# Optimization experiments

Hardware: AMD Instinct MI355X
Metric: run time of the kernel (lower is better)

Reference implementation:

```python
import jax, jax.numpy as jnp
import numpy as np

N_NODES = 100000
N_EDGES = 3200000
N_FEAT = 512
HIDDEN = 16
N_CLASS = 7


def gcn_conv(x, edge_index, W, b, n_nodes):
    """PyG GCNConv (add_self_loops=True, symmetric normalization).
    x: [N, F_in]; edge_index: [2, E] with row=source, col=target.
    """
    h = x @ W  # [N, F_out] -- linear transform before aggregation (F_out small)
    src, dst = edge_index[0], edge_index[1]
    # degree computed on target column (incl. self-loop), as in PyG gcn_norm
    deg = jax.ops.segment_sum(jnp.ones(src.shape[0], dtype=h.dtype), dst,
                              num_segments=n_nodes) + 1.0
    dinv = jax.lax.rsqrt(deg)  # deg >= 1 always (self-loops)
    norm = dinv[src] * dinv[dst]  # [E]
    msg = norm[:, None] * h[src]  # [E, F_out]
    agg = jax.ops.segment_sum(msg, dst, num_segments=n_nodes)
    # self-loop contribution: norm_ii = dinv_i^2
    agg = agg + (dinv * dinv)[:, None] * h
    return agg + b


def setup_inputs() -> dict:
    key = jax.random.key(0)
    k1, k2, k3, k4 = jax.random.split(key, 4)
    x = jax.random.normal(k1, (N_NODES, N_FEAT), dtype=jnp.float32)
    edge_index = jax.random.randint(k2, (2, N_EDGES), 0, N_NODES, dtype=jnp.int64)
    W1 = jax.random.normal(k3, (N_FEAT, HIDDEN), dtype=jnp.float32) * (1.0 / np.sqrt(N_FEAT))
    b1 = jnp.zeros((HIDDEN,), dtype=jnp.float32)
    W2 = jax.random.normal(k4, (HIDDEN, N_CLASS), dtype=jnp.float32) * (1.0 / np.sqrt(HIDDEN))
    b2 = jnp.zeros((N_CLASS,), dtype=jnp.float32)
    return {"x": x, "edge_index": edge_index, "W1": W1, "b1": b1, "W2": W2, "b2": b2}


def reference(x, edge_index, W1, b1, W2, b2):
    n = x.shape[0]
    h = gcn_conv(x, edge_index, W1, b1, n)
    h = jax.nn.relu(h)
    # F.dropout in eval mode is identity (deterministic reference)
    h = gcn_conv(h, edge_index, W2, b2, n)
    return jax.nn.log_softmax(h, axis=1)
```

## Files before the change

### kernel.cpp

```cpp
#include <hip/hip_runtime.h>
#include <math.h>


#define F_IN 512
#define HID  16
#define NCLS 7
#define NCHUNK 256
#define BK 256
#define NBMAX 400
#define CAP 9216
#define WT_STRIDE 516

static __device__ __forceinline__ float bf2f(unsigned short u) {
    union { unsigned int i; float f; } v; v.i = ((unsigned int)u) << 16; return v.f;
}
static __device__ __forceinline__ unsigned short f2bf(float f) {
    union { float f; unsigned int u; } v; v.f = f;
    unsigned int b = v.u;
    return (unsigned short)((b + 0x7FFFu + ((b >> 16) & 1u)) >> 16);
}

__global__ __launch_bounds__(256) void k_a1(const int* __restrict__ ei, int E, int perChunk,
                                            int nb, int* __restrict__ bh) {
    __shared__ int hist[NBMAX];
    for (int t = threadIdx.x; t < nb; t += 256) hist[t] = 0;
    __syncthreads();
    const int* dst = ei + E;
    int c = blockIdx.x;
    int s0 = c * perChunk;
    int s1 = min(s0 + perChunk, E);
    for (int e = s0 + threadIdx.x; e < s1; e += 256)
        atomicAdd(&hist[dst[e] >> 8], 1);
    __syncthreads();
    for (int t = threadIdx.x; t < nb; t += 256) bh[(size_t)c * nb + t] = hist[t];
}

__global__ __launch_bounds__(256) void k_a2a(int* __restrict__ bh, int nb,
                                             int* __restrict__ Tb) {
    __shared__ int sd[256];
    int b = blockIdx.x, tid = threadIdx.x;
    int v = bh[(size_t)tid * nb + b];
    sd[tid] = v;
    __syncthreads();
    for (int off = 1; off < 256; off <<= 1) {
        int t = (tid >= off) ? sd[tid - off] : 0;
        __syncthreads();
        sd[tid] += t;
        __syncthreads();
    }
    bh[(size_t)tid * nb + b] = sd[tid] - v;
    if (tid == 255) Tb[b] = sd[255];
}

__global__ __launch_bounds__(256) void k_a2b(const int* __restrict__ Tb, int nb,
                                             int* __restrict__ Bb) {
    __shared__ int sd[256];
    int tid = threadIdx.x;
    int carry = 0;
    for (int base = 0; base < nb; base += 256) {
        int v = (base + tid < nb) ? Tb[base + tid] : 0;
        sd[tid] = v;
        __syncthreads();
        for (int off = 1; off < 256; off <<= 1) {
            int t = (tid >= off) ? sd[tid - off] : 0;
            __syncthreads();
            sd[tid] += t;
            __syncthreads();
        }
        if (base + tid < nb) Bb[base + tid] = carry + sd[tid] - v;
        carry += sd[255];
        __syncthreads();
    }
}

__global__ __launch_bounds__(256) void k_a3(const int* __restrict__ ei, int E, int perChunk,
                                            int nb, const int* __restrict__ bh,
                                            const int* __restrict__ Bb,
                                            unsigned* __restrict__ part) {
    __shared__ int cur[NBMAX];
    __shared__ int baseL[NBMAX];
    int c = blockIdx.x;
    for (int t = threadIdx.x; t < nb; t += 256) {
        cur[t] = 0;
        baseL[t] = Bb[t] + bh[(size_t)c * nb + t];
    }
    __syncthreads();
    const int* src = ei;
    const int* dst = ei + E;
    int s0 = c * perChunk;
    int s1 = min(s0 + perChunk, E);
    for (int e = s0 + threadIdx.x; e < s1; e += 256) {
        int s = src[e], d = dst[e];
        int b = d >> 8;
        int r = atomicAdd(&cur[b], 1);
        part[baseL[b] + r] = ((unsigned)(d & (BK - 1)) << 20) | (unsigned)s;
    }
}

__global__ __launch_bounds__(256) void k_b(const unsigned* __restrict__ part,
                                           const int* __restrict__ Tb,
                                           const int* __restrict__ Bb,
                                           int* __restrict__ csr, int* __restrict__ cnt,
                                           int* __restrict__ offs, float* __restrict__ dinv,
                                           int N) {
    __shared__ unsigned eL[CAP];
    __shared__ int hist[BK], sd[BK], cur[BK];
    int b = blockIdx.x, tid = threadIdx.x;
    int base = Bb[b], ct = Tb[b];
    hist[tid] = 0;
    __syncthreads();
    for (int k = tid; k < ct; k += 256) {
        unsigned v = part[base + k];
        if (k < CAP) eL[k] = v;
        atomicAdd(&hist[v >> 20], 1);
    }
    __syncthreads();
    sd[tid] = hist[tid];
    __syncthreads();
    for (int off = 1; off < BK; off <<= 1) {
        int t = (tid >= off) ? sd[tid - off] : 0;
        __syncthreads();
        sd[tid] += t;
        __syncthreads();
    }
    {
        int h = hist[tid];
        int ex = sd[tid] - h;
        cur[tid] = ex;
        int node = b * BK + tid;
        if (node < N) {
            cnt[node] = h;
            offs[node] = base + ex;
            dinv[node] = rsqrtf((float)h + 1.0f);
        }
    }
    __syncthreads();
    for (int k = tid; k < ct; k += 256) {
        unsigned v = (k < CAP) ? eL[k] : part[base + k];
        int dl = (int)(v >> 20);
        int r = atomicAdd(&cur[dl], 1);
        csr[base + r] = (int)(v & 0xFFFFFu);
    }
}

__global__ __launch_bounds__(256) void k_gemm1(const float* __restrict__ x,
                                               const float* __restrict__ W1,
                                               const float* __restrict__ dinv,
                                               unsigned short* __restrict__ hs1b,
                                               int N) {
    __shared__ float wlT[HID * WT_STRIDE];

    int lane = threadIdx.x & 15;
    int g = threadIdx.x >> 4;
    int rbase = blockIdx.x * 64 + g * 4;

    const float* xp0 = x + (size_t)(rbase + 0 < N ? rbase + 0 : 0) * F_IN + 4 * lane;
    const float* xp1 = x + (size_t)(rbase + 1 < N ? rbase + 1 : 0) * F_IN + 4 * lane;
    const float* xp2 = x + (size_t)(rbase + 2 < N ? rbase + 2 : 0) * F_IN + 4 * lane;
    const float* xp3 = x + (size_t)(rbase + 3 < N ? rbase + 3 : 0) * F_IN + 4 * lane;

    float4 a0 = *(const float4*)(xp0);
    float4 a1 = *(const float4*)(xp1);
    float4 a2 = *(const float4*)(xp2);
    float4 a3 = *(const float4*)(xp3);

    {
        int j = threadIdx.x & 15;
        int k0 = threadIdx.x >> 4;
        for (int it = 0; it < F_IN / 16; ++it) {
            int k = k0 + 16 * it;
            wlT[j * WT_STRIDE + k] = W1[k * HID + j];
        }
    }
    __syncthreads();

    float acc[4][16];
#pragma unroll
    for (int r = 0; r < 4; ++r)
#pragma unroll
        for (int j = 0; j < 16; ++j) acc[r][j] = 0.0f;

    auto fma_block = [&](int p, const float4& A0, const float4& A1,
                         const float4& A2, const float4& A3) {
        const float* wb = &wlT[64 * p + 4 * lane];
#pragma unroll
        for (int j = 0; j < 16; ++j) {
            float4 w4 = *(const float4*)(wb + (size_t)j * WT_STRIDE);
            acc[0][j] = fmaf(A0.x, w4.x, fmaf(A0.y, w4.y, fmaf(A0.z, w4.z, fmaf(A0.w, w4.w, acc[0][j]))));
            acc[1][j] = fmaf(A1.x, w4.x, fmaf(A1.y, w4.y, fmaf(A1.z, w4.z, fmaf(A1.w, w4.w, acc[1][j]))));
            acc[2][j] = fmaf(A2.x, w4.x, fmaf(A2.y, w4.y, fmaf(A2.z, w4.z, fmaf(A2.w, w4.w, acc[2][j]))));
            acc[3][j] = fmaf(A3.x, w4.x, fmaf(A3.y, w4.y, fmaf(A3.z, w4.z, fmaf(A3.w, w4.w, acc[3][j]))));
        }
    };

#pragma unroll 1
    for (int p = 0; p < 7; ++p) {
        float4 n0 = *(const float4*)(xp0 + 64 * (p + 1));
        float4 n1 = *(const float4*)(xp1 + 64 * (p + 1));
        float4 n2 = *(const float4*)(xp2 + 64 * (p + 1));
        float4 n3 = *(const float4*)(xp3 + 64 * (p + 1));
        fma_block(p, a0, a1, a2, a3);
        a0 = n0; a1 = n1; a2 = n2; a3 = n3;
    }
    fma_block(7, a0, a1, a2, a3);

    bool b8 = (lane & 8) != 0, b4 = (lane & 4) != 0, b2 = (lane & 2) != 0, b1 = (lane & 1) != 0;
#pragma unroll
    for (int r = 0; r < 4; ++r) {
#pragma unroll
        for (int j = 0; j < 8; ++j) {
            float lo = acc[r][j], hi = acc[r][j + 8];
            float keep = b8 ? hi : lo;
            float send = b8 ? lo : hi;
            acc[r][j] = keep + __shfl_xor(send, 8, 16);
        }
#pragma unroll
        for (int j = 0; j < 4; ++j) {
            float lo = acc[r][j], hi = acc[r][j + 4];
            float keep = b4 ? hi : lo;
            float send = b4 ? lo : hi;
            acc[r][j] = keep + __shfl_xor(send, 4, 16);
        }
#pragma unroll
        for (int j = 0; j < 2; ++j) {
            float lo = acc[r][j], hi = acc[r][j + 2];
            float keep = b2 ? hi : lo;
            float send = b2 ? lo : hi;
            acc[r][j] = keep + __shfl_xor(send, 2, 16);
        }
        {
            float lo = acc[r][0], hi = acc[r][1];
            float keep = b1 ? hi : lo;
            float send = b1 ? lo : hi;
            acc[r][0] = keep + __shfl_xor(send, 1, 16);
        }
        int row = rbase + r;
        if (row < N)
            hs1b[(size_t)row * HID + lane] = f2bf(dinv[row] * acc[r][0]);
    }
}

__global__ __launch_bounds__(256) void k_agg1(const int* __restrict__ csr,
                                              const int* __restrict__ offs,
                                              const int* __restrict__ cnt,
                                              const float* __restrict__ dinv,
                                              const unsigned* __restrict__ hs1u,
                                              const float* __restrict__ b1,
                                              const float* __restrict__ W2,
                                              float* __restrict__ hs2p, int N) {
    int lane = threadIdx.x & 7;
    int i = blockIdx.x * 32 + (threadIdx.x >> 3);
    float w2a[NCLS], w2b[NCLS];
#pragma unroll
    for (int c = 0; c < NCLS; c++) {
        w2a[c] = W2[(2 * lane) * NCLS + c];
        w2b[c] = W2[(2 * lane + 1) * NCLS + c];
    }
    float b1a = b1[2 * lane], b1b = b1[2 * lane + 1];
    if (i >= N) return;
    int start = offs[i], cn = cnt[i];
    unsigned su = hs1u[(size_t)i * 8 + lane];
    float accA = __uint_as_float(su << 16);
    float accB = __uint_as_float(su & 0xffff0000u);
    int full = cn & ~7;
    int rem = cn - full;
    int evn = csr[start + lane];
    for (int k = 0; k < full; k += 8) {
        int ev = evn;
        evn = csr[start + k + 8 + lane];
#pragma unroll
        for (int t = 0; t < 8; ++t) {
            int s = __shfl(ev, t, 8);
            unsigned u = hs1u[(size_t)s * 8 + lane];
            accA += __uint_as_float(u << 16);
            accB += __uint_as_float(u & 0xffff0000u);
        }
    }
    for (int t = 0; t < rem; ++t) {
        int s = __shfl(evn, t, 8);
        unsigned u = hs1u[(size_t)s * 8 + lane];
        accA += __uint_as_float(u << 16);
        accB += __uint_as_float(u & 0xffff0000u);
    }
    float dv = dinv[i];
    float vA = fmaf(dv, accA, b1a);
    float vB = fmaf(dv, accB, b1b);
    float hA = vA > 0.0f ? vA : 0.0f;
    float hB = vB > 0.0f ? vB : 0.0f;
    float res[NCLS];
#pragma unroll
    for (int c = 0; c < NCLS; c++) {
        float t = fmaf(hA, w2a[c], hB * w2b[c]);
#pragma unroll
        for (int w = 4; w >= 1; w >>= 1) t += __shfl_xor(t, w, 8);
        res[c] = t;
    }
    float o = res[0];
#pragma unroll
    for (int c = 1; c < NCLS; c++) o = (lane == c) ? res[c] : o;
    hs2p[(size_t)i * 8 + lane] = dv * o;
}

__global__ __launch_bounds__(256) void k_agg2(const int* __restrict__ csr,
                                              const int* __restrict__ offs,
                                              const int* __restrict__ cnt,
                                              const float* __restrict__ dinv,
                                              const float* __restrict__ hs2p,
                                              const float* __restrict__ b2,
                                              float* __restrict__ out, int N) {
    int lane = threadIdx.x & 7;
    int i = blockIdx.x * 32 + (threadIdx.x >> 3);
    if (i >= N) return;
    int start = offs[i], cn = cnt[i];
    float acc = hs2p[(size_t)i * 8 + lane];
    int full = cn & ~7;
    int rem = cn - full;
    int evn = csr[start + lane];
    for (int k = 0; k < full; k += 8) {
        int ev = evn;
        evn = csr[start + k + 8 + lane];
#pragma unroll
        for (int t = 0; t < 8; ++t) {
            int s = __shfl(ev, t, 8);
            acc += hs2p[(size_t)s * 8 + lane];
        }
    }
    for (int t = 0; t < rem; ++t) {
        int s = __shfl(evn, t, 8);
        acc += hs2p[(size_t)s * 8 + lane];
    }
    int cc = lane < NCLS ? lane : NCLS - 1;
    float v = fmaf(dinv[i], acc, b2[cc]);
    float vm = (lane < NCLS) ? v : -INFINITY;
    float m = vm;
#pragma unroll
    for (int w = 4; w >= 1; w >>= 1) m = fmaxf(m, __shfl_xor(m, w, 8));
    float e = (lane < NCLS) ? expf(v - m) : 0.0f;
    float ssum = e;
#pragma unroll
    for (int w = 4; w >= 1; w >>= 1) ssum += __shfl_xor(ssum, w, 8);
    if (lane < NCLS) out[(size_t)i * NCLS + lane] = v - m - logf(ssum);
}

extern "C" void kernel_launch(void* const* d_in, const int* in_sizes, int n_in,
                              void* d_out, int out_size, void* d_ws, size_t ws_size,
                              hipStream_t stream) {
    const float* x  = (const float*)d_in[0];
    const int*   ei = (const int*)d_in[1];
    const float* W1 = (const float*)d_in[2];
    const float* b1 = (const float*)d_in[3];
    const float* W2 = (const float*)d_in[4];
    const float* b2 = (const float*)d_in[5];
    float* out = (float*)d_out;

    const int N = in_sizes[0] / F_IN;
    const int E = in_sizes[1] / 2;
    const int nb = (N + BK - 1) / BK;
    const int perChunk = (E + NCHUNK - 1) / NCHUNK;

    unsigned* w = (unsigned*)d_ws;
    auto al4 = [](size_t v) { return (v + 3) & ~(size_t)3; };
    size_t o = 0;
    unsigned*       part = w + o;
    float*          hs2p = (float*)(w + o);     o = al4(o + E);
    int*            csr  = (int*)(w + o);       o = al4(o + E + 16);
    unsigned short* hs1b = (unsigned short*)(w + o); o = al4(o + (size_t)N * HID / 2);
    float*          dinv = (float*)(w + o);     o = al4(o + N);
    int*            cnt  = (int*)(w + o);       o = al4(o + N);
    int*            offs = (int*)(w + o);       o = al4(o + N);
    int*            bh   = (int*)(w + o);       o = al4(o + (size_t)NCHUNK * nb);
    int*            Tb   = (int*)(w + o);       o = al4(o + nb);
    int*            Bb   = (int*)(w + o);

    k_a1<<<NCHUNK, 256, 0, stream>>>(ei, E, perChunk, nb, bh);
    k_a2a<<<nb, 256, 0, stream>>>(bh, nb, Tb);
    k_a2b<<<1, 256, 0, stream>>>(Tb, nb, Bb);
    k_a3<<<NCHUNK, 256, 0, stream>>>(ei, E, perChunk, nb, bh, Bb, part);
    k_b<<<nb, 256, 0, stream>>>(part, Tb, Bb, csr, cnt, offs, dinv, N);
    k_gemm1<<<(N + 63) / 64, 256, 0, stream>>>(x, W1, dinv, hs1b, N);
    k_agg1<<<(N + 31) / 32, 256, 0, stream>>>(csr, offs, cnt, dinv,
                                              (const unsigned*)hs1b, b1, W2, hs2p, N);
    k_agg2<<<(N + 31) / 32, 256, 0, stream>>>(csr, offs, cnt, dinv, hs2p, b2, out, N);
}
```

Before: 448.5 us.

## Overlap the dense GEMM with CSR-build kernels by co-launching GEMM blocks

Measured after the change: 474.9 us. 1.06x slower.

```diff
diff --git a/kernel.cpp b/kernel.cpp
--- a/kernel.cpp
+++ b/kernel.cpp
@@ -10,23 +10,115 @@
 #define NBMAX 400
 #define CAP 9216
 #define WT_STRIDE 516
-
-static __device__ __forceinline__ float bf2f(unsigned short u) {
-    union { unsigned int i; float f; } v; v.i = ((unsigned int)u) << 16; return v.f;
-}
+#define SM_GEMM (HID * WT_STRIDE * 4)
+#define SM_KB   (CAP * 4 + 3 * BK * 4)
+
 static __device__ __forceinline__ unsigned short f2bf(float f) {
     union { float f; unsigned int u; } v; v.f = f;
     unsigned int b = v.u;
     return (unsigned short)((b + 0x7FFFu + ((b >> 16) & 1u)) >> 16);
 }
 
-__global__ __launch_bounds__(256) void k_a1(const int* __restrict__ ei, int E, int perChunk,
-                                            int nb, int* __restrict__ bh) {
-    __shared__ int hist[NBMAX];
+
+static __device__ void gemm_body(int gb, const float* __restrict__ x,
+                                 const float* __restrict__ W1,
+                                 unsigned short* __restrict__ hs1b, int N,
+                                 float* wlT) {
+    int lane = threadIdx.x & 15;
+    int g = threadIdx.x >> 4;
+    int rbase = gb * 64 + g * 4;
+
+    const float* xp0 = x + (size_t)(rbase + 0 < N ? rbase + 0 : 0) * F_IN + 4 * lane;
+    const float* xp1 = x + (size_t)(rbase + 1 < N ? rbase + 1 : 0) * F_IN + 4 * lane;
+    const float* xp2 = x + (size_t)(rbase + 2 < N ? rbase + 2 : 0) * F_IN + 4 * lane;
+    const float* xp3 = x + (size_t)(rbase + 3 < N ? rbase + 3 : 0) * F_IN + 4 * lane;
+
+    float4 a0 = *(const float4*)(xp0);
+    float4 a1 = *(const float4*)(xp1);
+    float4 a2 = *(const float4*)(xp2);
+    float4 a3 = *(const float4*)(xp3);
+
+    {
+        int j = threadIdx.x & 15;
+        int k0 = threadIdx.x >> 4;
+        for (int it = 0; it < F_IN / 16; ++it) {
+            int k = k0 + 16 * it;
+            wlT[j * WT_STRIDE + k] = W1[k * HID + j];
+        }
+    }
+    __syncthreads();
+
+    float acc[4][16];
+#pragma unroll
+    for (int r = 0; r < 4; ++r)
+#pragma unroll
+        for (int j = 0; j < 16; ++j) acc[r][j] = 0.0f;
+
+    auto fma_block = [&](int p, const float4& A0, const float4& A1,
+                         const float4& A2, const float4& A3) {
+        const float* wb = &wlT[64 * p + 4 * lane];
+#pragma unroll
+        for (int j = 0; j < 16; ++j) {
+            float4 w4 = *(const float4*)(wb + (size_t)j * WT_STRIDE);
+            acc[0][j] = fmaf(A0.x, w4.x, fmaf(A0.y, w4.y, fmaf(A0.z, w4.z, fmaf(A0.w, w4.w, acc[0][j]))));
+            acc[1][j] = fmaf(A1.x, w4.x, fmaf(A1.y, w4.y, fmaf(A1.z, w4.z, fmaf(A1.w, w4.w, acc[1][j]))));
+            acc[2][j] = fmaf(A2.x, w4.x, fmaf(A2.y, w4.y, fmaf(A2.z, w4.z, fmaf(A2.w, w4.w, acc[2][j]))));
+            acc[3][j] = fmaf(A3.x, w4.x, fmaf(A3.y, w4.y, fmaf(A3.z, w4.z, fmaf(A3.w, w4.w, acc[3][j]))));
+        }
+    };
+
+#pragma unroll 1
+    for (int p = 0; p < 7; ++p) {
+        float4 n0 = *(const float4*)(xp0 + 64 * (p + 1));
+        float4 n1 = *(const float4*)(xp1 + 64 * (p + 1));
+        float4 n2 = *(const float4*)(xp2 + 64 * (p + 1));
+        float4 n3 = *(const float4*)(xp3 + 64 * (p + 1));
+        fma_block(p, a0, a1, a2, a3);
+        a0 = n0; a1 = n1; a2 = n2; a3 = n3;
+    }
+    fma_block(7, a0, a1, a2, a3);
+
+    bool b8 = (lane & 8) != 0, b4 = (lane & 4) != 0, b2 = (lane & 2) != 0, b1 = (lane & 1) != 0;
+#pragma unroll
+    for (int r = 0; r < 4; ++r) {
+#pragma unroll
+        for (int j = 0; j < 8; ++j) {
+            float lo = acc[r][j], hi = acc[r][j + 8];
+            float keep = b8 ? hi : lo;
+            float send = b8 ? lo : hi;
+            acc[r][j] = keep + __shfl_xor(send, 8, 16);
+        }
+#pragma unroll
+        for (int j = 0; j < 4; ++j) {
+            float lo = acc[r][j], hi = acc[r][j + 4];
+            float keep = b4 ? hi : lo;
+            float send = b4 ? lo : hi;
+            acc[r][j] = keep + __shfl_xor(send, 4, 16);
+        }
+#pragma unroll
+        for (int j = 0; j < 2; ++j) {
+            float lo = acc[r][j], hi = acc[r][j + 2];
+            float keep = b2 ? hi : lo;
+            float send = b2 ? lo : hi;
+            acc[r][j] = keep + __shfl_xor(send, 2, 16);
+        }
+        {
+            float lo = acc[r][0], hi = acc[r][1];
+            float keep = b1 ? hi : lo;
+            float send = b1 ? lo : hi;
+            acc[r][0] = keep + __shfl_xor(send, 1, 16);
+        }
+        int row = rbase + r;
+        if (row < N)
+            hs1b[(size_t)row * HID + lane] = f2bf(acc[r][0]);
+    }
+}
+
+static __device__ void a1_body(int c, const int* __restrict__ ei, int E, int perChunk,
+                               int nb, int* __restrict__ bh, int* hist) {
     for (int t = threadIdx.x; t < nb; t += 256) hist[t] = 0;
     __syncthreads();
     const int* dst = ei + E;
-    int c = blockIdx.x;
     int s0 = c * perChunk;
     int s1 = min(s0 + perChunk, E);
     for (int e = s0 + threadIdx.x; e < s1; e += 256)
@@ -35,10 +127,9 @@
     for (int t = threadIdx.x; t < nb; t += 256) bh[(size_t)c * nb + t] = hist[t];
 }
 
-__global__ __launch_bounds__(256) void k_a2a(int* __restrict__ bh, int nb,
-                                             int* __restrict__ Tb) {
-    __shared__ int sd[256];
-    int b = blockIdx.x, tid = threadIdx.x;
+static __device__ void a2a_body(int b, int* __restrict__ bh, int nb,
+                                int* __restrict__ Tb, int* sd) {
+    int tid = threadIdx.x;
     int v = bh[(size_t)tid * nb + b];
     sd[tid] = v;
     __syncthreads();
@@ -52,10 +143,11 @@
     if (tid == 255) Tb[b] = sd[255];
 }
 
-__global__ __launch_bounds__(256) void k_a2b(const int* __restrict__ Tb, int nb,
-                                             int* __restrict__ Bb) {
-    __shared__ int sd[256];
+static __device__ void a2b_body(const int* __restrict__ Tb, int nb,
+                                int* __restrict__ Bb, int* sd,
+                                int* __restrict__ csr, int E) {
     int tid = threadIdx.x;
+    if (tid < 16) csr[E + tid] = 0;
     int carry = 0;
     for (int base = 0; base < nb; base += 256) {
         int v = (base + tid < nb) ? Tb[base + tid] : 0;
@@ -73,13 +165,11 @@
     }
 }
 
-__global__ __launch_bounds__(256) void k_a3(const int* __restrict__ ei, int E, int perChunk,
-                                            int nb, const int* __restrict__ bh,
-                                            const int* __restrict__ Bb,
-                                            unsigned* __restrict__ part) {
-    __shared__ int cur[NBMAX];
-    __shared__ int baseL[NBMAX];
-    int c = blockIdx.x;
+static __device__ void a3_body(int c, const int* __restrict__ ei, int E, int perChunk,
+                               int nb, const int* __restrict__ bh,
+                               const int* __restrict__ Bb,
+                               unsigned* __restrict__ part,
+                               int* cur, int* baseL) {
     for (int t = threadIdx.x; t < nb; t += 256) {
         cur[t] = 0;
         baseL[t] = Bb[t] + bh[(size_t)c * nb + t];
@@ -97,15 +187,13 @@
     }
 }
 
-__global__ __launch_bounds__(256) void k_b(const unsigned* __restrict__ part,
-                                           const int* __restrict__ Tb,
-                                           const int* __restrict__ Bb,
-                                           int* __restrict__ csr, int* __restrict__ cnt,
-                                           int* __restrict__ offs, float* __restrict__ dinv,
-                                           int N) {
-    __shared__ unsigned eL[CAP];
-    __shared__ int hist[BK], sd[BK], cur[BK];
-    int b = blockIdx.x, tid = threadIdx.x;
+static __device__ void kb_body(int b, const unsigned* __restrict__ part,
+                               const int* __restrict__ Tb,
+                               const int* __restrict__ Bb,
+                               int* __restrict__ csr, int* __restrict__ cnt,
+                               int* __restrict__ offs, float* __restrict__ dinv,
+                               int N, unsigned* eL, int* hist, int* sd, int* cur) {
+    int tid = threadIdx.x;
     int base = Bb[b], ct = Tb[b];
     hist[tid] = 0;
     __syncthreads();
@@ -143,101 +231,80 @@
     }
 }
 
-__global__ __launch_bounds__(256) void k_gemm1(const float* __restrict__ x,
-                                               const float* __restrict__ W1,
-                                               const float* __restrict__ dinv,
-                                               unsigned short* __restrict__ hs1b,
-                                               int N) {
-    __shared__ float wlT[HID * WT_STRIDE];
-
-    int lane = threadIdx.x & 15;
-    int g = threadIdx.x >> 4;
-    int rbase = blockIdx.x * 64 + g * 4;
-
-    const float* xp0 = x + (size_t)(rbase + 0 < N ? rbase + 0 : 0) * F_IN + 4 * lane;
-    const float* xp1 = x + (size_t)(rbase + 1 < N ? rbase + 1 : 0) * F_IN + 4 * lane;
-    const float* xp2 = x + (size_t)(rbase + 2 < N ? rbase + 2 : 0) * F_IN + 4 * lane;
-    const float* xp3 = x + (size_t)(rbase + 3 < N ? rbase + 3 : 0) * F_IN + 4 * lane;
-
-    float4 a0 = *(const float4*)(xp0);
-    float4 a1 = *(const float4*)(xp1);
-    float4 a2 = *(const float4*)(xp2);
-    float4 a3 = *(const float4*)(xp3);
-
-    {
-        int j = threadIdx.x & 15;
-        int k0 = threadIdx.x >> 4;
-        for (int it = 0; it < F_IN / 16; ++it) {
-            int k = k0 + 16 * it;
-            wlT[j * WT_STRIDE + k] = W1[k * HID + j];
-        }
-    }
-    __syncthreads();
-
-    float acc[4][16];
-#pragma unroll
-    for (int r = 0; r < 4; ++r)
-#pragma unroll
-        for (int j = 0; j < 16; ++j) acc[r][j] = 0.0f;
-
-    auto fma_block = [&](int p, const float4& A0, const float4& A1,
-                         const float4& A2, const float4& A3) {
-        const float* wb = &wlT[64 * p + 4 * lane];
-#pragma unroll
-        for (int j = 0; j < 16; ++j) {
-            float4 w4 = *(const float4*)(wb + (size_t)j * WT_STRIDE);
-            acc[0][j] = fmaf(A0.x, w4.x, fmaf(A0.y, w4.y, fmaf(A0.z, w4.z, fmaf(A0.w, w4.w, acc[0][j]))));
-            acc[1][j] = fmaf(A1.x, w4.x, fmaf(A1.y, w4.y, fmaf(A1.z, w4.z, fmaf(A1.w, w4.w, acc[1][j]))));
-            acc[2][j] = fmaf(A2.x, w4.x, fmaf(A2.y, w4.y, fmaf(A2.z, w4.z, fmaf(A2.w, w4.w, acc[2][j]))));
-            acc[3][j] = fmaf(A3.x, w4.x, fmaf(A3.y, w4.y, fmaf(A3.z, w4.z, fmaf(A3.w, w4.w, acc[3][j]))));
-        }
-    };
-
-#pragma unroll 1
-    for (int p = 0; p < 7; ++p) {
-        float4 n0 = *(const float4*)(xp0 + 64 * (p + 1));
-        float4 n1 = *(const float4*)(xp1 + 64 * (p + 1));
-        float4 n2 = *(const float4*)(xp2 + 64 * (p + 1));
-        float4 n3 = *(const float4*)(xp3 + 64 * (p + 1));
-        fma_block(p, a0, a1, a2, a3);
-        a0 = n0; a1 = n1; a2 = n2; a3 = n3;
-    }
-    fma_block(7, a0, a1, a2, a3);
-
-    bool b8 = (lane & 8) != 0, b4 = (lane & 4) != 0, b2 = (lane & 2) != 0, b1 = (lane & 1) != 0;
-#pragma unroll
-    for (int r = 0; r < 4; ++r) {
-#pragma unroll
-        for (int j = 0; j < 8; ++j) {
-            float lo = acc[r][j], hi = acc[r][j + 8];
-            float keep = b8 ? hi : lo;
-            float send = b8 ? lo : hi;
-            acc[r][j] = keep + __shfl_xor(send, 8, 16);
-        }
-#pragma unroll
-        for (int j = 0; j < 4; ++j) {
-            float lo = acc[r][j], hi = acc[r][j + 4];
-            float keep = b4 ? hi : lo;
-            float send = b4 ? lo : hi;
-            acc[r][j] = keep + __shfl_xor(send, 4, 16);
-        }
-#pragma unroll
-        for (int j = 0; j < 2; ++j) {
-            float lo = acc[r][j], hi = acc[r][j + 2];
-            float keep = b2 ? hi : lo;
-            float send = b2 ? lo : hi;
-            acc[r][j] = keep + __shfl_xor(send, 2, 16);
-        }
-        {
-            float lo = acc[r][0], hi = acc[r][1];
-            float keep = b1 ? hi : lo;
-            float send = b1 ? lo : hi;
-            acc[r][0] = keep + __shfl_xor(send, 1, 16);
-        }
-        int row = rbase + r;
-        if (row < N)
-            hs1b[(size_t)row * HID + lane] = f2bf(dinv[row] * acc[r][0]);
-    }
+
+__global__ __launch_bounds__(256) void k_f1(const int* __restrict__ ei, int E, int perChunk,
+                                            int nb, int* __restrict__ bh,
+                                            const float* __restrict__ x,
+                                            const float* __restrict__ W1,
+                                            unsigned short* __restrict__ hs1b, int N,
+                                            int gBase) {
+    __shared__ __align__(16) unsigned char sm[SM_GEMM];
+    if ((int)blockIdx.x < NCHUNK)
+        a1_body(blockIdx.x, ei, E, perChunk, nb, bh, (int*)sm);
+    else
+        gemm_body(gBase + (int)blockIdx.x - NCHUNK, x, W1, hs1b, N, (float*)sm);
+}
+
+__global__ __launch_bounds__(256) void k_f2(int* __restrict__ bh, int nb,
+                                            int* __restrict__ Tb,
+                                            const float* __restrict__ x,
+                                            const float* __restrict__ W1,
+                                            unsigned short* __restrict__ hs1b, int N,
+                                            int gBase) {
+    __shared__ __align__(16) unsigned char sm[SM_GEMM];
+    if ((int)blockIdx.x < nb)
+        a2a_body(blockIdx.x, bh, nb, Tb, (int*)sm);
+    else
+        gemm_body(gBase + (int)blockIdx.x - nb, x, W1, hs1b, N, (float*)sm);
+}
+
+__global__ __launch_bounds__(256) void k_f3(const int* __restrict__ Tb, int nb,
+                                            int* __restrict__ Bb,
+                                            int* __restrict__ csr, int E,
+                                            const float* __restrict__ x,
+                                            const float* __restrict__ W1,
+                                            unsigned short* __restrict__ hs1b, int N,
+                                            int gBase) {
+    __shared__ __align__(16) unsigned char sm[SM_GEMM];
+    if ((int)blockIdx.x < 1)
+        a2b_body(Tb, nb, Bb, (int*)sm, csr, E);
+    else
+        gemm_body(gBase + (int)blockIdx.x - 1, x, W1, hs1b, N, (float*)sm);
+}
+
+__global__ __launch_bounds__(256) void k_f4(const int* __restrict__ ei, int E, int perChunk,
+                                            int nb, const int* __restrict__ bh,
+                                            const int* __restrict__ Bb,
+                                            unsigned* __restrict__ part,
+                                            const float* __restrict__ x,
+                                            const float* __restrict__ W1,
+                                            unsigned short* __restrict__ hs1b, int N,
+                                            int gBase) {
+    __shared__ __align__(16) unsigned char sm[SM_GEMM];
+    if ((int)blockIdx.x < NCHUNK)
+        a3_body(blockIdx.x, ei, E, perChunk, nb, bh, Bb, part,
+                (int*)sm, (int*)(sm + 4 * NBMAX));
+    else
+        gemm_body(gBase + (int)blockIdx.x - NCHUNK, x, W1, hs1b, N, (float*)sm);
+}
+
+__global__ __launch_bounds__(256) void k_f5(const unsigned* __restrict__ part,
+                                            const int* __restrict__ Tb,
+                                            const int* __restrict__ Bb,
+                                            int* __restrict__ csr, int* __restrict__ cnt,
+                                            int* __restrict__ offs, float* __restrict__ dinv,
+                                            int nb,
+                                            const float* __restrict__ x,
+                                            const float* __restrict__ W1,
+                                            unsigned short* __restrict__ hs1b, int N,
+                                            int gBase) {
+    __shared__ __align__(16) unsigned char sm[SM_KB];
+    if ((int)blockIdx.x < nb)
+        kb_body(blockIdx.x, part, Tb, Bb, csr, cnt, offs, dinv, N,
+                (unsigned*)sm, (int*)(sm + 4 * CAP),
+                (int*)(sm + 4 * CAP + 4 * BK), (int*)(sm + 4 * CAP + 8 * BK));
+    else
+        gemm_body(gBase + (int)blockIdx.x - nb, x, W1, hs1b, N, (float*)sm);
 }
 
 __global__ __launch_bounds__(256) void k_agg1(const int* __restrict__ csr,
@@ -259,32 +326,36 @@
     float b1a = b1[2 * lane], b1b = b1[2 * lane + 1];
     if (i >= N) return;
     int start = offs[i], cn = cnt[i];
+    float dvi = dinv[i];
     unsigned su = hs1u[(size_t)i * 8 + lane];
-    float accA = __uint_as_float(su << 16);
-    float accB = __uint_as_float(su & 0xffff0000u);
+    float accA = dvi * __uint_as_float(su << 16);
+    float accB = dvi * __uint_as_float(su & 0xffff0000u);
     int full = cn & ~7;
     int rem = cn - full;
     int evn = csr[start + lane];
+    float dvn = dinv[evn];
     for (int k = 0; k < full; k += 8) {
-        int ev = evn;
+        int ev = evn; float dvv = dvn;
         evn = csr[start + k + 8 + lane];
+        dvn = dinv[evn];
 #pragma unroll
         for (int t = 0; t < 8; ++t) {
             int s = __shfl(ev, t, 8);
+            float ds = __shfl(dvv, t, 8);
             unsigned u = hs1u[(size_t)s * 8 + lane];
-            accA += __uint_as_float(u << 16);
-            accB += __uint_as_float(u & 0xffff0000u);
+            accA = fmaf(ds, __uint_as_float(u << 16), accA);
+            accB = fmaf(ds, __uint_as_float(u & 0xffff0000u), accB);
         }
     }
     for (int t = 0; t < rem; ++t) {
         int s = __shfl(evn, t, 8);
+        float ds = __shfl(dvn, t, 8);
         unsigned u = hs1u[(size_t)s * 8 + lane];
-        accA += __uint_as_float(u << 16);
-        accB += __uint_as_float(u & 0xffff0000u);
-    }
-    float dv = dinv[i];
-    float vA = fmaf(dv, accA, b1a);
-    float vB = fmaf(dv, accB, b1b);
+        accA = fmaf(ds, __uint_as_float(u << 16), accA);
+        accB = fmaf(ds, __uint_as_float(u & 0xffff0000u), accB);
+    }
+    float vA = fmaf(dvi, accA, b1a);
+    float vB = fmaf(dvi, accB, b1b);
     float hA = vA > 0.0f ? vA : 0.0f;
     float hB = vB > 0.0f ? vB : 0.0f;
     float res[NCLS];
@@ -298,7 +369,7 @@
     float o = res[0];
 #pragma unroll
     for (int c = 1; c < NCLS; c++) o = (lane == c) ? res[c] : o;
-    hs2p[(size_t)i * 8 + lane] = dv * o;
+    hs2p[(size_t)i * 8 + lane] = dvi * o;
 }
 
 __global__ __launch_bounds__(256) void k_agg2(const int* __restrict__ csr,
@@ -358,6 +429,15 @@
     const int nb = (N + BK - 1) / BK;
     const int perChunk = (E + NCHUNK - 1) / NCHUNK;
 
+    const int gemmNB = (N + 63) / 64;
+    const int g1 = gemmNB * 13 / 100;
+    const int g2 = gemmNB * 12 / 100;
+    const int g3 = gemmNB * 3 / 100;
+    const int g4 = gemmNB * 32 / 100;
+    const int g5 = gemmNB - g1 - g2 - g3 - g4;
+    const int gb1 = 0, gb2 = g1, gb3 = g1 + g2, gb4 = g1 + g2 + g3,
+              gb5 = g1 + g2 + g3 + g4;
+
     unsigned* w = (unsigned*)d_ws;
     auto al4 = [](size_t v) { return (v + 3) & ~(size_t)3; };
     size_t o = 0;
@@ -372,12 +452,11 @@
     int*            Tb   = (int*)(w + o);       o = al4(o + nb);
     int*            Bb   = (int*)(w + o);
 
-    k_a1<<<NCHUNK, 256, 0, stream>>>(ei, E, perChunk, nb, bh);
-    k_a2a<<<nb, 256, 0, stream>>>(bh, nb, Tb);
-    k_a2b<<<1, 256, 0, stream>>>(Tb, nb, Bb);
-    k_a3<<<NCHUNK, 256, 0, stream>>>(ei, E, perChunk, nb, bh, Bb, part);
-    k_b<<<nb, 256, 0, stream>>>(part, Tb, Bb, csr, cnt, offs, dinv, N);
-    k_gemm1<<<(N + 63) / 64, 256, 0, stream>>>(x, W1, dinv, hs1b, N);
+    k_f1<<<NCHUNK + g1, 256, 0, stream>>>(ei, E, perChunk, nb, bh, x, W1, hs1b, N, gb1);
+    k_f2<<<nb + g2, 256, 0, stream>>>(bh, nb, Tb, x, W1, hs1b, N, gb2);
+    k_f3<<<1 + g3, 256, 0, stream>>>(Tb, nb, Bb, csr, E, x, W1, hs1b, N, gb3);
+    k_f4<<<NCHUNK + g4, 256, 0, stream>>>(ei, E, perChunk, nb, bh, Bb, part, x, W1, hs1b, N, gb4);
+    k_f5<<<nb + g5, 256, 0, stream>>>(part, Tb, Bb, csr, cnt, offs, dinv, nb, x, W1, hs1b, N, gb5);
     k_agg1<<<(N + 31) / 32, 256, 0, stream>>>(csr, offs, cnt, dinv,
                                               (const unsigned*)hs1b, b1, W2, hs2p, N);
     k_agg2<<<(N + 31) / 32, 256, 0, stream>>>(csr, offs, cnt, dinv, hs2p, b2, out, N);
```
